# Kernel tuning notes

Measured on AMD Instinct MI355X. Metric: run time of the kernel, lower is better.

## Reference

```python
import jax, jax.numpy as jnp
import numpy as np

RMS_EPS = 1.1920929e-07  # torch.finfo(float32).eps, used by F.rms_norm default


def _rms_norm(x):
    # RMSNorm over last dim, no learnable weight (matches F.rms_norm(x, (d,)))
    ms = jnp.mean(jnp.square(x), axis=-1, keepdims=True)
    return x * jax.lax.rsqrt(ms + RMS_EPS)


def _apply_rotary(x, cos, sin):
    # x: [N, H, D]; cos/sin: [N, 1, D//2]
    d = x.shape[-1] // 2
    x1, x2 = x[..., :d], x[..., d:]
    y1 = x1 * cos + x2 * sin
    y2 = -x1 * sin + x2 * cos
    return jnp.concatenate([y1, y2], axis=-1)


def setup_inputs() -> dict:
    key = jax.random.key(0)
    k1, k2, k3 = jax.random.split(key, 3)
    n_embd, n_head, head_dim = 1024, 16, 64
    n_seqs, seqlen = 4, 1024
    N = n_seqs * seqlen
    x = jax.random.normal(k1, (N, n_embd), dtype=jnp.float32)
    Wqkv = jax.random.normal(k2, (3 * n_embd, n_embd), dtype=jnp.float32) * (n_embd ** -0.5)
    Wo = jax.random.normal(k3, (n_embd, n_embd), dtype=jnp.float32) * (n_embd ** -0.5)
    # standard rotary caches over positions [0, seqlen)
    inv_freq = 1.0 / (10000.0 ** (np.arange(0, head_dim // 2) / (head_dim // 2)))
    pos = np.arange(seqlen)[:, None] * inv_freq[None, :]  # [seqlen, head_dim//2]
    cos_cache = jnp.asarray(np.cos(pos), dtype=jnp.float32)
    sin_cache = jnp.asarray(np.sin(pos), dtype=jnp.float32)
    cu_seqlens = jnp.arange(n_seqs + 1, dtype=jnp.int32) * seqlen
    position_ids = jnp.tile(jnp.arange(seqlen, dtype=jnp.int32), n_seqs)
    return {"x": x, "Wqkv": Wqkv, "Wo": Wo, "cos_cache": cos_cache,
            "sin_cache": sin_cache, "cu_seqlens": cu_seqlens,
            "position_ids": position_ids, "max_seqlen": seqlen}


def reference(x, Wqkv, Wo, cos_cache, sin_cache, cu_seqlens, position_ids, max_seqlen):
    N, n_embd = x.shape
    S = int(max_seqlen)
    B = N // S  # equal-length packed sequences
    n_head = 16
    head_dim = n_embd // n_head

    qkv = (x @ Wqkv.T).reshape(N, 3, n_head, head_dim)
    cos = cos_cache[position_ids][:, None, :]  # [N,1,D/2]
    sin = sin_cache[position_ids][:, None, :]
    q = _rms_norm(_apply_rotary(qkv[:, 0], cos, sin))
    k = _rms_norm(_apply_rotary(qkv[:, 1], cos, sin))
    v = qkv[:, 2]

    q = q.reshape(B, S, n_head, head_dim)
    k = k.reshape(B, S, n_head, head_dim)
    v = v.reshape(B, S, n_head, head_dim)

    scale = head_dim ** -0.5
    scores = jnp.einsum('bqhd,bkhd->bhqk', q, k) * scale
    causal = jnp.tril(jnp.ones((S, S), dtype=bool))
    scores = jnp.where(causal, scores, jnp.finfo(scores.dtype).min)
    probs = jax.nn.softmax(scores, axis=-1)
    out = jnp.einsum('bhqk,bkhd->bqhd', probs, v).reshape(N, n_embd)
    return out @ Wo.T
```

## Files before the change

kernel.cpp:

```cpp
#include <hip/hip_runtime.h>
#include <hip/hip_bf16.h>

typedef unsigned short u16;
typedef __bf16 bf16x8 __attribute__((ext_vector_type(8)));
typedef float f32x4 __attribute__((ext_vector_type(4)));
typedef u16 u16x8 __attribute__((ext_vector_type(8)));
typedef u16 u16x4 __attribute__((ext_vector_type(4)));

__device__ __forceinline__ u16 f2bf(float f) {
    unsigned u = __builtin_bit_cast(unsigned, f);
    unsigned r = u + 0x7FFFu + ((u >> 16) & 1u);
    return (u16)(r >> 16);
}
__device__ __forceinline__ float bf2f(u16 h) {
    return __builtin_bit_cast(float, (unsigned)h << 16);
}
__device__ __forceinline__ unsigned cvt_pk_bf16(float lo, float hi) {
    unsigned r;
    asm("v_cvt_pk_bf16_f32 %0, %1, %2" : "=v"(r) : "v"(lo), "v"(hi));
    return r;
}
__device__ __forceinline__ void gload16(const void* g, void* l) {
    __builtin_amdgcn_global_load_lds((const __attribute__((address_space(1))) void*)g,
                                     (__attribute__((address_space(3))) void*)l, 16, 0, 0);
}

__global__ __launch_bounds__(256) void cvt_all(const float* __restrict__ x,
                                               const float* __restrict__ wqkv,
                                               const float* __restrict__ wo,
                                               u16* __restrict__ dst, int n0, int n1) {
    int i = (blockIdx.x * 256 + threadIdx.x) * 4;
    const float* src;
    if (i < n0)            src = x + i;
    else if (i < n0 + n1)  src = wqkv + (i - n0);
    else                   src = wo + (i - n0 - n1);
    float4 v = *(const float4*)src;
    u16x4 o;
    o[0] = f2bf(v.x); o[1] = f2bf(v.y); o[2] = f2bf(v.z); o[3] = f2bf(v.w);
    *(u16x4*)(dst + i) = o;
}

template <int BM, int BN, int WR, int WC, bool OUT_BF16>
__global__ __launch_bounds__(WR * WC * 64, (WR * WC == 8) ? 4 : 2)
void gemm_pipe(const u16* __restrict__ A,
               const u16* __restrict__ Bt,
               void* __restrict__ C,
               int M, int N, int K) {
    constexpr int NW = WR * WC;
    constexpr int MR = BM / WR / 16, NR = BN / WC / 16;
    constexpr int MGS = (MR >= 4) ? 4 : MR;
    constexpr int CA = BM / 8, CB = BN / 8;
    constexpr int CAW = CA / NW, CBW = CB / NW;
    constexpr int NLD = CAW + CBW;

    __shared__ u16 lA[2][BM * 64];
    __shared__ u16 lB[2][BN * 64];

    const int tid = threadIdx.x, lane = tid & 63, w = tid >> 6;
    const int wr = w / WC, wc = w % WC;
    const int lr = lane & 15, lg = lane >> 4;
    const int sw = (lr & 7) << 4;
    const int bm = blockIdx.x * BM, bn = blockIdx.y * BN;
    const int jr = lane >> 3;
    const int scbe = ((((lane & 7) * 16) ^ (jr << 4)) >> 1);
    const int nTk = K >> 6;

    f32x4 acc[MR][NR];
#pragma unroll
    for (int i = 0; i < MR; i++)
#pragma unroll
        for (int j = 0; j < NR; j++) acc[i][j] = (f32x4){0.f, 0.f, 0.f, 0.f};

    const u16* aSrc = A + (size_t)bm * K + scbe;
    const u16* bSrc = Bt + (size_t)bn * K + scbe;

#define STAGEP(p_, t_)                                                           \
    {                                                                            \
        _Pragma("unroll") for (int q = 0; q < CAW; q++) {                        \
            int ck = w * CAW + q;                                                \
            gload16(aSrc + (size_t)(ck * 8 + jr) * K + (t_) * 64,                \
                    &lA[p_][ck * 512]);                                          \
        }                                                                        \
        _Pragma("unroll") for (int q = 0; q < CBW; q++) {                        \
            int ck = w * CBW + q;                                                \
            gload16(bSrc + (size_t)(ck * 8 + jr) * K + (t_) * 64,                \
                    &lB[p_][ck * 512]);                                          \
        }                                                                        \
    }

    STAGEP(0, 0);

    for (int t = 0; t < nTk; t++) {
        const int p = t & 1;
        if (t + 1 < nTk) {
            STAGEP(p ^ 1, t + 1);
            if constexpr (NLD == 3)
                asm volatile("s_waitcnt vmcnt(3)" ::: "memory");
            else if constexpr (NLD == 5)
                asm volatile("s_waitcnt vmcnt(5)" ::: "memory");
            else if constexpr (NLD == 6)
                asm volatile("s_waitcnt vmcnt(6)" ::: "memory");
            else if constexpr (NLD == 7)
                asm volatile("s_waitcnt vmcnt(7)" ::: "memory");
            else if constexpr (NLD == 8)
                asm volatile("s_waitcnt vmcnt(8)" ::: "memory");
            else if constexpr (NLD == 10)
                asm volatile("s_waitcnt vmcnt(10)" ::: "memory");
            else
                asm volatile("s_waitcnt vmcnt(0)" ::: "memory");
        } else {
            asm volatile("s_waitcnt vmcnt(0)" ::: "memory");
        }
        __builtin_amdgcn_s_barrier();
        __builtin_amdgcn_sched_barrier(0);

        const char* pa = (const char*)&lA[p][0] + (size_t)(wr * MR * 16) * 128;
        const char* pb = (const char*)&lB[p][0] + (size_t)(wc * NR * 16) * 128;
#pragma unroll
        for (int ks = 0; ks < 2; ks++) {
            bf16x8 bfr[NR];
#pragma unroll
            for (int j = 0; j < NR; j++)
                bfr[j] = *(const bf16x8*)(pb + (j * 16 + lr) * 128 +
                                          ((ks * 64 + lg * 16) ^ sw));
#pragma unroll
            for (int mg = 0; mg < MR; mg += MGS) {
                bf16x8 af[MGS];
#pragma unroll
                for (int i = 0; i < MGS; i++)
                    af[i] = *(const bf16x8*)(pa + ((mg + i) * 16 + lr) * 128 +
                                             ((ks * 64 + lg * 16) ^ sw));
                __builtin_amdgcn_s_setprio(1);
#pragma unroll
                for (int i = 0; i < MGS; i++)
#pragma unroll
                    for (int j = 0; j < NR; j++)
                        acc[mg + i][j] = __builtin_amdgcn_mfma_f32_16x16x32_bf16(
                            af[i], bfr[j], acc[mg + i][j], 0, 0, 0);
                __builtin_amdgcn_s_setprio(0);
            }
        }
        __builtin_amdgcn_s_barrier();
    }
#undef STAGEP

    const int row0 = bm + wr * MR * 16, col0 = bn + wc * NR * 16;
#pragma unroll
    for (int i = 0; i < MR; i++)
#pragma unroll
        for (int j = 0; j < NR; j++)
#pragma unroll
            for (int r = 0; r < 4; r++) {
                int m = row0 + i * 16 + lg * 4 + r;
                int n = col0 + j * 16 + lr;
                float v = acc[i][j][r];
                if (OUT_BF16)
                    ((u16*)C)[(size_t)m * N + n] = f2bf(v);
                else
                    ((float*)C)[(size_t)m * N + n] = v;
            }
}

__global__ __launch_bounds__(256) void rope_trans(u16* __restrict__ qkv,
                                                  const float* __restrict__ cosc,
                                                  const float* __restrict__ sinc,
                                                  const int* __restrict__ pos_ids,
                                                  u16* __restrict__ vT, int S, int nbRope) {
    __shared__ u16 lt[64][72];
    const int bid = blockIdx.x;
    const int tid = threadIdx.x;
    if (bid < nbRope) {
        int idx = bid * 4 + (tid >> 6);
        int lane = tid & 63;
        int token = idx >> 4;
        int h = idx & 15;
        u16* p = qkv + (size_t)token * 3072 + 1024 + h * 64;
        float x = bf2f(p[lane]);
        float xp = __shfl_xor(x, 32);
        int pos = pos_ids[token];
        int j = lane & 31;
        float c = cosc[pos * 32 + j], s = sinc[pos * 32 + j];
        float y = (lane < 32) ? (x * c + xp * s) : (x * c - xp * s);
        float ss = y * y;
#pragma unroll
        for (int m = 1; m < 64; m <<= 1) ss += __shfl_xor(ss, m);
        float r = rsqrtf(ss * (1.0f / 64.0f) + 1.1920929e-07f);
        p[lane] = f2bf(y * r);
    } else {
        int t = bid - nbRope;
        int nsc = S >> 6;
        int bh = t / nsc;
        int b = bh >> 4, h = bh & 15;
        int s0 = (t - bh * nsc) * 64;
        {
            int s = tid >> 2, dp = (tid & 3) * 16;
            const u16* src = qkv + (size_t)(b * S + s0 + s) * 3072 + 2048 + h * 64 + dp;
            u16x8 v0 = *(const u16x8*)src;
            u16x8 v1 = *(const u16x8*)(src + 8);
#pragma unroll
            for (int i = 0; i < 8; i++) lt[s][dp + i] = v0[i];
#pragma unroll
            for (int i = 0; i < 8; i++) lt[s][dp + 8 + i] = v1[i];
        }
        __syncthreads();
        {
            int d = tid >> 2, sp = (tid & 3) * 16;
            u16x8 o0, o1;
#pragma unroll
            for (int i = 0; i < 8; i++) o0[i] = lt[sp + i][d];
#pragma unroll
            for (int i = 0; i < 8; i++) o1[i] = lt[sp + 8 + i][d];
            u16* dst = vT + ((size_t)bh * 64 + d) * S + s0 + sp;
            *(u16x8*)dst = o0;
            *(u16x8*)(dst + 8) = o1;
        }
    }
}

__global__ __launch_bounds__(256) void attn_fwd(const u16* __restrict__ qkv,
                                                const u16* __restrict__ vT,
                                                const float* __restrict__ cosc,
                                                const float* __restrict__ sinc,
                                                u16* __restrict__ out, int S) {
    const int bh = blockIdx.x, b = bh >> 4, h = bh & 15;
    const int tid = threadIdx.x, lane = tid & 63, w = tid >> 6;
    const int lr = lane & 15, lg = lane >> 4;
    const int sw = (lr & 7) << 4;

    const int nq = S >> 6;
    const int i1 = blockIdx.y;
    const int i2 = (nq - 1) - i1;
    const int n1 = i1 + 1, ntot = n1 + i2 + 1;

    __shared__ u16 lK[3][64 * 64];
    __shared__ u16 lVt[3][64 * 64];
    __shared__ u16 lP[4][16 * 64];

    const int jr = lane >> 3;
    const int cbyte = (lane & 7) * 16;
    const int scb = cbyte ^ (jr << 4);
    const int rowA = w * 16 + jr, rowB = rowA + 8;
    const u16* kSrc = qkv + 1024 + h * 64 + (scb >> 1);
    const u16* vSrc = vT + (size_t)bh * 64 * S + (scb >> 1);

#define KVOF(x_) ((((x_) < n1) ? (x_) : (x_) - n1) * 64)

#define STAGE(bufi, kv0_)                                                        \
    {                                                                            \
        const u16* kb = kSrc + (size_t)(b * S + (kv0_)) * 3072;                  \
        const u16* vb = vSrc + (kv0_);                                           \
        gload16(kb + (size_t)rowA * 3072, &lK[bufi][(w * 2) * 512]);             \
        gload16(kb + (size_t)rowB * 3072, &lK[bufi][(w * 2 + 1) * 512]);         \
        gload16(vb + (size_t)rowA * S, &lVt[bufi][(w * 2) * 512]);               \
        gload16(vb + (size_t)rowB * S, &lVt[bufi][(w * 2 + 1) * 512]);           \
    }

    bf16x8 bQ[2];
    f32x4 oT[4];
    float lrun;

#define LOADQ(tile_)                                                             \
    {                                                                            \
        const int qrow = (tile_)*64 + w * 16 + lr;                               \
        const u16* qp = qkv + (size_t)(b * S + qrow) * 3072 + h * 64;            \
        u16x8 t0 = *(const u16x8*)(qp + lg * 8);                                 \
        u16x8 t1 = *(const u16x8*)(qp + 32 + lg * 8);                            \
        const float* cc = cosc + qrow * 32 + lg * 8;                             \
        const float* sc = sinc + qrow * 32 + lg * 8;                             \
        float y0[8], y1[8], ss = 0.f;                                            \
        _Pragma("unroll") for (int i = 0; i < 8; i++) {                          \
            float c = cc[i], s = sc[i];                                          \
            float x1 = bf2f(t0[i]), x2 = bf2f(t1[i]);                            \
            y0[i] = x1 * c + x2 * s;                                             \
            y1[i] = x2 * c - x1 * s;                                             \
            ss += y0[i] * y0[i] + y1[i] * y1[i];                                 \
        }                                                                        \
        ss += __shfl_xor(ss, 16);                                                \
        ss += __shfl_xor(ss, 32);                                                \
        float sc2 = rsqrtf(ss * (1.0f / 64.0f) + 1.1920929e-07f) * 0.18033688f;  \
        bf16x8 a0, a1;                                                           \
        _Pragma("unroll") for (int i = 0; i < 8; i++) {                          \
            a0[i] = (__bf16)(y0[i] * sc2);                                       \
            a1[i] = (__bf16)(y1[i] * sc2);                                       \
        }                                                                        \
        bQ[0] = a0; bQ[1] = a1;                                                  \
    }

    STAGE(0, 0);
    if (1 < ntot) STAGE(1, KVOF(1));
    LOADQ(i1);
#pragma unroll
    for (int df = 0; df < 4; df++) oT[df] = (f32x4){0.f, 0.f, 0.f, 0.f};
    lrun = 0.f;

    int buf = 0;
    for (int s = 0; s < ntot; s++) {
        const int tile = (s < n1) ? i1 : i2;
        const int kv0 = KVOF(s);
        if (s + 1 < ntot)
            asm volatile("s_waitcnt vmcnt(4)" ::: "memory");
        else
            asm volatile("s_waitcnt vmcnt(0)" ::: "memory");
        __builtin_amdgcn_s_barrier();
        __builtin_amdgcn_sched_barrier(0);
        if (s + 2 < ntot) {
            int wb = buf + 2; if (wb >= 3) wb -= 3;
            STAGE(wb, KVOF(s + 2));
        }
        const bool diag = (s == n1 - 1) || (s == ntot - 1);

        f32x4 st[4];
#pragma unroll
        for (int kf = 0; kf < 4; kf++) {
            const char* kb = (const char*)&lK[buf][0] + (kf * 16 + lr) * 128;
            bf16x8 k0 = *(const bf16x8*)(kb + ((lg * 16) ^ sw));
            bf16x8 k1 = *(const bf16x8*)(kb + ((64 + lg * 16) ^ sw));
            f32x4 z = (f32x4){0.f, 0.f, 0.f, 0.f};
            z = __builtin_amdgcn_mfma_f32_16x16x32_bf16(k0, bQ[0], z, 0, 0, 0);
            st[kf] = __builtin_amdgcn_mfma_f32_16x16x32_bf16(k1, bQ[1], z, 0, 0, 0);
        }

        if (diag) {
            const int qg = tile * 64 + w * 16 + lr;
#pragma unroll
            for (int kf = 0; kf < 4; kf++)
#pragma unroll
                for (int r = 0; r < 4; r++) {
                    int kvg = kv0 + kf * 16 + lg * 4 + r;
                    if (kvg > qg) st[kf][r] = -3.0e38f;
                }
        }
        float ps = 0.f;
#pragma unroll
        for (int kf = 0; kf < 4; kf++)
#pragma unroll
            for (int r = 0; r < 4; r++) {
                float p = exp2f(st[kf][r]);
                st[kf][r] = p;
                ps += p;
            }
        lrun += ps;

        {
            char* pb = (char*)&lP[w][0] + lr * 128;
#pragma unroll
            for (int kf = 0; kf < 4; kf++) {
                uint2 pk;
                pk.x = cvt_pk_bf16(st[kf][0], st[kf][1]);
                pk.y = cvt_pk_bf16(st[kf][2], st[kf][3]);
                *(uint2*)(pb + ((kf * 32 + lg * 8) ^ sw)) = pk;
            }
        }

#pragma unroll
        for (int kc = 0; kc < 2; kc++) {
            bf16x8 bp = *(const bf16x8*)((const char*)&lP[w][0] + lr * 128 +
                                         ((kc * 64 + lg * 16) ^ sw));
#pragma unroll
            for (int df = 0; df < 4; df++) {
                bf16x8 av = *(const bf16x8*)((const char*)&lVt[buf][0] +
                                             (df * 16 + lr) * 128 +
                                             ((kc * 64 + lg * 16) ^ sw));
                oT[df] = __builtin_amdgcn_mfma_f32_16x16x32_bf16(av, bp, oT[df], 0, 0, 0);
            }
        }

        if (diag) {
            float tot = lrun;
            tot += __shfl_xor(tot, 16);
            tot += __shfl_xor(tot, 32);
            float inv = 1.0f / tot;
            u16* op = out + (size_t)(b * S + tile * 64 + w * 16 + lr) * 1024 +
                      h * 64 + lg * 4;
#pragma unroll
            for (int df = 0; df < 4; df++) {
                u16x4 o;
#pragma unroll
                for (int r = 0; r < 4; r++) o[r] = f2bf(oT[df][r] * inv);
                *(u16x4*)(op + df * 16) = o;
            }
            if (s != ntot - 1) {
                LOADQ(i2);
#pragma unroll
                for (int df = 0; df < 4; df++) oT[df] = (f32x4){0.f, 0.f, 0.f, 0.f};
                lrun = 0.f;
            }
        }
        buf++; if (buf == 3) buf = 0;
    }
#undef STAGE
#undef LOADQ
#undef KVOF
}

extern "C" void kernel_launch(void* const* d_in, const int* in_sizes, int n_in,
                              void* d_out, int out_size, void* d_ws, size_t ws_size,
                              hipStream_t stream) {
    const float* x     = (const float*)d_in[0];
    const float* Wqkv  = (const float*)d_in[1];
    const float* Wo    = (const float*)d_in[2];
    const float* cosc  = (const float*)d_in[3];
    const float* sinc  = (const float*)d_in[4];
    const int* pos_ids = (const int*)d_in[6];

    const int E = 1024, H = 16;
    int S = in_sizes[3] / 32;
    int N = in_sizes[0] / E;
    int B = N / S;

    char* ws = (char*)d_ws;
    u16* xb    = (u16*)ws;
    u16* wqkvb = (u16*)(ws + (size_t)N * E * 2);
    u16* wob   = (u16*)(ws + (size_t)N * E * 2 + (size_t)3 * E * E * 2);
    u16* qkvb  = (u16*)(ws + (size_t)N * E * 2 + (size_t)4 * E * E * 2);
    u16* vTb   = (u16*)(ws + (size_t)N * E * 2 + (size_t)4 * E * E * 2 + (size_t)N * 3 * E * 2);
    u16* aout  = xb;

    int n0 = N * E, n1 = 3 * E * E, n2 = E * E;
    cvt_all<<<(n0 + n1 + n2) / 1024, 256, 0, stream>>>(x, Wqkv, Wo, xb, n0, n1);

    gemm_pipe<128, 192, 2, 4, true><<<dim3(N / 128, 3 * E / 192), 512, 0, stream>>>(
        xb, wqkvb, qkvb, N, 3 * E, E);

    int nbRope = N * H / 4;
    int nbTrans = B * H * (S / 64);
    rope_trans<<<nbRope + nbTrans, 256, 0, stream>>>(qkvb, cosc, sinc, pos_ids, vTb, S, nbRope);

    attn_fwd<<<dim3(B * H, S / 128), 256, 0, stream>>>(qkvb, vTb, cosc, sinc, aout, S);

    gemm_pipe<64, 128, 2, 4, false><<<dim3(N / 64, E / 128), 512, 0, stream>>>(
        aout, wob, d_out, N, E, E);
}
```

Baseline: 99.38 us.

## Fuse rotary and RMS norm for Q and K into QKV GEMM epilogue

The QKV GEMM epilogue now applies rotary embedding and RMS norm to the Q and K columns, with the softmax scale folded into Q, before writing bf16. The separate rope pass over K and the per-tile Q rope/norm inside attention are removed, leaving a standalone V-transpose kernel. This saves a read-modify-write of K and repeated Q normalisation work. In exchange the QKV GEMM tiling changes to 128x128 with a 4x2 wave layout so each wave spans one 64-wide head, which alters occupancy and the load pipeline depth.

Measured after the change: 96.76 us. 1.03x faster.

```diff
diff --git a/kernel.cpp b/kernel.cpp
--- a/kernel.cpp
+++ b/kernel.cpp
@@ -40,18 +40,22 @@
     *(u16x4*)(dst + i) = o;
 }
 
-template <int BM, int BN, int WR, int WC, bool OUT_BF16>
+template <int BM, int BN, int WR, int WC, bool OUT_BF16, bool FUSE_ROPE>
 __global__ __launch_bounds__(WR * WC * 64, (WR * WC == 8) ? 4 : 2)
 void gemm_pipe(const u16* __restrict__ A,
                const u16* __restrict__ Bt,
                void* __restrict__ C,
-               int M, int N, int K) {
+               int M, int N, int K,
+               const float* __restrict__ cosc,
+               const float* __restrict__ sinc,
+               const int* __restrict__ pos_ids) {
     constexpr int NW = WR * WC;
     constexpr int MR = BM / WR / 16, NR = BN / WC / 16;
     constexpr int MGS = (MR >= 4) ? 4 : MR;
     constexpr int CA = BM / 8, CB = BN / 8;
     constexpr int CAW = CA / NW, CBW = CB / NW;
     constexpr int NLD = CAW + CBW;
+    static_assert(!FUSE_ROPE || NR == 4, "FUSE_ROPE needs 64-col wave span");
 
     __shared__ u16 lA[2][BM * 64];
     __shared__ u16 lB[2][BN * 64];
@@ -96,12 +100,12 @@
             STAGEP(p ^ 1, t + 1);
             if constexpr (NLD == 3)
                 asm volatile("s_waitcnt vmcnt(3)" ::: "memory");
+            else if constexpr (NLD == 4)
+                asm volatile("s_waitcnt vmcnt(4)" ::: "memory");
             else if constexpr (NLD == 5)
                 asm volatile("s_waitcnt vmcnt(5)" ::: "memory");
             else if constexpr (NLD == 6)
                 asm volatile("s_waitcnt vmcnt(6)" ::: "memory");
-            else if constexpr (NLD == 7)
-                asm volatile("s_waitcnt vmcnt(7)" ::: "memory");
             else if constexpr (NLD == 8)
                 asm volatile("s_waitcnt vmcnt(8)" ::: "memory");
             else if constexpr (NLD == 10)
@@ -145,6 +149,51 @@
 #undef STAGEP
 
     const int row0 = bm + wr * MR * 16, col0 = bn + wc * NR * 16;
+
+    if constexpr (FUSE_ROPE) {
+        u16* Cb = (u16*)C;
+        if (col0 < 2048) {
+            const float qs = (col0 < 1024) ? 0.18033688f : 1.0f;
+#pragma unroll
+            for (int i = 0; i < MR; i++) {
+#pragma unroll
+                for (int r = 0; r < 4; r++) {
+                    const int m = row0 + i * 16 + lg * 4 + r;
+                    const int pos = pos_ids[m];
+                    const float c0 = cosc[pos * 32 + lr],      s0 = sinc[pos * 32 + lr];
+                    const float c1 = cosc[pos * 32 + 16 + lr], s1 = sinc[pos * 32 + 16 + lr];
+                    const float x0 = acc[i][0][r], x1 = acc[i][1][r];
+                    const float x2 = acc[i][2][r], x3 = acc[i][3][r];
+                    const float y0 = x0 * c0 + x2 * s0;
+                    const float y2 = x2 * c0 - x0 * s0;
+                    const float y1 = x1 * c1 + x3 * s1;
+                    const float y3 = x3 * c1 - x1 * s1;
+                    float ss = y0 * y0 + y1 * y1 + y2 * y2 + y3 * y3;
+                    ss += __shfl_xor(ss, 1);
+                    ss += __shfl_xor(ss, 2);
+                    ss += __shfl_xor(ss, 4);
+                    ss += __shfl_xor(ss, 8);
+                    const float scl = rsqrtf(ss * (1.0f / 64.0f) + 1.1920929e-07f) * qs;
+                    u16* cp = Cb + (size_t)m * N + col0 + lr;
+                    cp[0]  = f2bf(y0 * scl);
+                    cp[16] = f2bf(y1 * scl);
+                    cp[32] = f2bf(y2 * scl);
+                    cp[48] = f2bf(y3 * scl);
+                }
+            }
+        } else {
+#pragma unroll
+            for (int i = 0; i < MR; i++)
+#pragma unroll
+                for (int j = 0; j < NR; j++)
+#pragma unroll
+                    for (int r = 0; r < 4; r++)
+                        Cb[(size_t)(row0 + i * 16 + lg * 4 + r) * N + col0 + j * 16 + lr] =
+                            f2bf(acc[i][j][r]);
+        }
+        return;
+    }
+
 #pragma unroll
     for (int i = 0; i < MR; i++)
 #pragma unroll
@@ -161,66 +210,40 @@
             }
 }
 
-__global__ __launch_bounds__(256) void rope_trans(u16* __restrict__ qkv,
-                                                  const float* __restrict__ cosc,
-                                                  const float* __restrict__ sinc,
-                                                  const int* __restrict__ pos_ids,
-                                                  u16* __restrict__ vT, int S, int nbRope) {
+__global__ __launch_bounds__(256) void trans_v(const u16* __restrict__ qkv,
+                                               u16* __restrict__ vT, int S) {
     __shared__ u16 lt[64][72];
-    const int bid = blockIdx.x;
     const int tid = threadIdx.x;
-    if (bid < nbRope) {
-        int idx = bid * 4 + (tid >> 6);
-        int lane = tid & 63;
-        int token = idx >> 4;
-        int h = idx & 15;
-        u16* p = qkv + (size_t)token * 3072 + 1024 + h * 64;
-        float x = bf2f(p[lane]);
-        float xp = __shfl_xor(x, 32);
-        int pos = pos_ids[token];
-        int j = lane & 31;
-        float c = cosc[pos * 32 + j], s = sinc[pos * 32 + j];
-        float y = (lane < 32) ? (x * c + xp * s) : (x * c - xp * s);
-        float ss = y * y;
-#pragma unroll
-        for (int m = 1; m < 64; m <<= 1) ss += __shfl_xor(ss, m);
-        float r = rsqrtf(ss * (1.0f / 64.0f) + 1.1920929e-07f);
-        p[lane] = f2bf(y * r);
-    } else {
-        int t = bid - nbRope;
-        int nsc = S >> 6;
-        int bh = t / nsc;
-        int b = bh >> 4, h = bh & 15;
-        int s0 = (t - bh * nsc) * 64;
-        {
-            int s = tid >> 2, dp = (tid & 3) * 16;
-            const u16* src = qkv + (size_t)(b * S + s0 + s) * 3072 + 2048 + h * 64 + dp;
-            u16x8 v0 = *(const u16x8*)src;
-            u16x8 v1 = *(const u16x8*)(src + 8);
-#pragma unroll
-            for (int i = 0; i < 8; i++) lt[s][dp + i] = v0[i];
-#pragma unroll
-            for (int i = 0; i < 8; i++) lt[s][dp + 8 + i] = v1[i];
-        }
-        __syncthreads();
-        {
-            int d = tid >> 2, sp = (tid & 3) * 16;
-            u16x8 o0, o1;
-#pragma unroll
-            for (int i = 0; i < 8; i++) o0[i] = lt[sp + i][d];
-#pragma unroll
-            for (int i = 0; i < 8; i++) o1[i] = lt[sp + 8 + i][d];
-            u16* dst = vT + ((size_t)bh * 64 + d) * S + s0 + sp;
-            *(u16x8*)dst = o0;
-            *(u16x8*)(dst + 8) = o1;
-        }
+    int nsc = S >> 6;
+    int bh = blockIdx.x / nsc;
+    int b = bh >> 4, h = bh & 15;
+    int s0 = (blockIdx.x - bh * nsc) * 64;
+    {
+        int s = tid >> 2, dp = (tid & 3) * 16;
+        const u16* src = qkv + (size_t)(b * S + s0 + s) * 3072 + 2048 + h * 64 + dp;
+        u16x8 v0 = *(const u16x8*)src;
+        u16x8 v1 = *(const u16x8*)(src + 8);
+#pragma unroll
+        for (int i = 0; i < 8; i++) lt[s][dp + i] = v0[i];
+#pragma unroll
+        for (int i = 0; i < 8; i++) lt[s][dp + 8 + i] = v1[i];
+    }
+    __syncthreads();
+    {
+        int d = tid >> 2, sp = (tid & 3) * 16;
+        u16x8 o0, o1;
+#pragma unroll
+        for (int i = 0; i < 8; i++) o0[i] = lt[sp + i][d];
+#pragma unroll
+        for (int i = 0; i < 8; i++) o1[i] = lt[sp + 8 + i][d];
+        u16* dst = vT + ((size_t)bh * 64 + d) * S + s0 + sp;
+        *(u16x8*)dst = o0;
+        *(u16x8*)(dst + 8) = o1;
     }
 }
 
 __global__ __launch_bounds__(256) void attn_fwd(const u16* __restrict__ qkv,
                                                 const u16* __restrict__ vT,
-                                                const float* __restrict__ cosc,
-                                                const float* __restrict__ sinc,
                                                 u16* __restrict__ out, int S) {
     const int bh = blockIdx.x, b = bh >> 4, h = bh & 15;
     const int tid = threadIdx.x, lane = tid & 63, w = tid >> 6;
@@ -261,29 +284,9 @@
 
 #define LOADQ(tile_)                                                             \
     {                                                                            \
-        const int qrow = (tile_)*64 + w * 16 + lr;                               \
-        const u16* qp = qkv + (size_t)(b * S + qrow) * 3072 + h * 64;            \
-        u16x8 t0 = *(const u16x8*)(qp + lg * 8);                                 \
-        u16x8 t1 = *(const u16x8*)(qp + 32 + lg * 8);                            \
-        const float* cc = cosc + qrow * 32 + lg * 8;                             \
-        const float* sc = sinc + qrow * 32 + lg * 8;                             \
-        float y0[8], y1[8], ss = 0.f;                                            \
-        _Pragma("unroll") for (int i = 0; i < 8; i++) {                          \
-            float c = cc[i], s = sc[i];                                          \
-            float x1 = bf2f(t0[i]), x2 = bf2f(t1[i]);                            \
-            y0[i] = x1 * c + x2 * s;                                             \
-            y1[i] = x2 * c - x1 * s;                                             \
-            ss += y0[i] * y0[i] + y1[i] * y1[i];                                 \
-        }                                                                        \
-        ss += __shfl_xor(ss, 16);                                                \
-        ss += __shfl_xor(ss, 32);                                                \
-        float sc2 = rsqrtf(ss * (1.0f / 64.0f) + 1.1920929e-07f) * 0.18033688f;  \
-        bf16x8 a0, a1;                                                           \
-        _Pragma("unroll") for (int i = 0; i < 8; i++) {                          \
-            a0[i] = (__bf16)(y0[i] * sc2);                                       \
-            a1[i] = (__bf16)(y1[i] * sc2);                                       \
-        }                                                                        \
-        bQ[0] = a0; bQ[1] = a1;                                                  \
+        const u16* qp = qkv + (size_t)(b * S + (tile_)*64 + w * 16 + lr) * 3072 + h * 64; \
+        bQ[0] = *(const bf16x8*)(qp + lg * 8);                                   \
+        bQ[1] = *(const bf16x8*)(qp + 32 + lg * 8);                              \
     }
 
     STAGE(0, 0);
@@ -419,15 +422,13 @@
     int n0 = N * E, n1 = 3 * E * E, n2 = E * E;
     cvt_all<<<(n0 + n1 + n2) / 1024, 256, 0, stream>>>(x, Wqkv, Wo, xb, n0, n1);
 
-    gemm_pipe<128, 192, 2, 4, true><<<dim3(N / 128, 3 * E / 192), 512, 0, stream>>>(
-        xb, wqkvb, qkvb, N, 3 * E, E);
-
-    int nbRope = N * H / 4;
-    int nbTrans = B * H * (S / 64);
-    rope_trans<<<nbRope + nbTrans, 256, 0, stream>>>(qkvb, cosc, sinc, pos_ids, vTb, S, nbRope);
-
-    attn_fwd<<<dim3(B * H, S / 128), 256, 0, stream>>>(qkvb, vTb, cosc, sinc, aout, S);
-
-    gemm_pipe<64, 128, 2, 4, false><<<dim3(N / 64, E / 128), 512, 0, stream>>>(
-        aout, wob, d_out, N, E, E);
-}
+    gemm_pipe<128, 128, 4, 2, true, true><<<dim3(N / 128, 3 * E / 128), 512, 0, stream>>>(
+        xb, wqkvb, qkvb, N, 3 * E, E, cosc, sinc, pos_ids);
+
+    trans_v<<<B * H * (S / 64), 256, 0, stream>>>(qkvb, vTb, S);
+
+    attn_fwd<<<dim3(B * H, S / 128), 256, 0, stream>>>(qkvb, vTb, aout, S);
+
+    gemm_pipe<64, 128, 2, 4, false, false><<<dim3(N / 64, E / 128), 512, 0, stream>>>(
+        aout, wob, d_out, N, E, E, nullptr, nullptr, nullptr);
+}
```
